# Kernel tuning notes

Measured on AMD Instinct MI355X. Metric: run time of the kernel, lower is better.

Reference implementation:

```python
import jax, jax.numpy as jnp
import numpy as np

N = 50000
E = 600000
IN_DIM = 256
H1, H2, H3 = 128, 64, 64
HEADS = 8


def _add_self_loops(edge_index, edge_weight=None):
    loop = jnp.arange(N, dtype=edge_index.dtype)
    src = jnp.concatenate([edge_index[0], loop])
    dst = jnp.concatenate([edge_index[1], loop])
    if edge_weight is None:
        return src, dst, None
    ew = jnp.concatenate([edge_weight, jnp.ones((N,), edge_weight.dtype)])
    return src, dst, ew


def gcn_conv(x, edge_index, edge_weight, W, b):
    # PyG GCNConv: add self-loops (weight 1), symmetric normalization, scatter-add.
    src, dst, ew = _add_self_loops(edge_index, edge_weight)
    deg = jax.ops.segment_sum(ew, dst, num_segments=N)          # [N]
    dinv = jnp.where(deg > 0, jax.lax.rsqrt(jnp.maximum(deg, 1e-12)), 0.0)
    coeff = dinv[src] * ew * dinv[dst]                          # [E+N]
    h = x @ W                                                    # [N, out]
    out = jax.ops.segment_sum(coeff[:, None] * h[src], dst, num_segments=N)
    return out + b


def gat_conv(x, edge_index, W, att_src, att_dst, b):
    # PyG GATConv, heads=HEADS, concat=False (mean over heads), leaky_relu slope 0.2.
    src, dst, _ = _add_self_loops(edge_index)
    C = W.shape[1] // HEADS
    h = (x @ W).reshape(N, HEADS, C)                             # [N,H,C]
    a_s = jnp.sum(h * att_src, axis=-1)                          # [N,H]
    a_d = jnp.sum(h * att_dst, axis=-1)                          # [N,H]
    e = jax.nn.leaky_relu(a_s[src] + a_d[dst], negative_slope=0.2)  # [E',H]
    # scatter-softmax over edges sharing a destination
    m = jax.ops.segment_max(e, dst, num_segments=N)              # [N,H]
    p = jnp.exp(e - m[dst])
    s = jax.ops.segment_sum(p, dst, num_segments=N)              # [N,H]
    alpha = p / (s[dst] + 1e-16)                                 # [E',H]
    out = jax.ops.segment_sum(alpha[:, :, None] * h[src], dst, num_segments=N)  # [N,H,C]
    return jnp.mean(out, axis=1) + b


def setup_inputs() -> dict:
    key = jax.random.key(0)
    ks = jax.random.split(key, 12)
    x = jax.random.normal(ks[0], (N, IN_DIM), dtype=jnp.float32)
    edge_index = jax.random.randint(ks[1], (2, E), 0, N, dtype=jnp.int32)
    edge_weight = jax.random.uniform(ks[2], (E,), dtype=jnp.float32)
    def glorot(k, shape):
        fan = shape[0] + shape[-1]
        return jax.random.normal(k, shape, dtype=jnp.float32) * np.sqrt(2.0 / fan)
    return {
        "x": x, "edge_index": edge_index, "edge_weight": edge_weight,
        "gc1_w": glorot(ks[3], (IN_DIM, H1)), "gc1_b": jnp.zeros((H1,), jnp.float32),
        "gat_w": glorot(ks[4], (H1, HEADS * H2)),
        "att_src": glorot(ks[5], (HEADS, H2)), "att_dst": glorot(ks[6], (HEADS, H2)),
        "gat_b": jnp.zeros((H2,), jnp.float32),
        "gc2_w": glorot(ks[7], (H2, H3)), "gc2_b": jnp.zeros((H3,), jnp.float32),
        "fc_w": glorot(ks[8], (H3, 1)), "fc_b": jnp.zeros((1,), jnp.float32),
    }


def reference(x, edge_index, edge_weight, gc1_w, gc1_b, gat_w, att_src, att_dst,
              gat_b, gc2_w, gc2_b, fc_w, fc_b):
    # dropout is inference no-op
    h = jax.nn.relu(gcn_conv(x, edge_index, edge_weight, gc1_w, gc1_b))
    h = jax.nn.relu(gat_conv(h, edge_index, gat_w, att_src, att_dst, gat_b))
    h = jax.nn.relu(gcn_conv(h, edge_index, edge_weight, gc2_w, gc2_b))
    return h @ fc_w + fc_b                                       # [N,1]
```

## Files before the change

kernel.cpp:

```cpp
#include <hip/hip_runtime.h>
#include <hip/hip_bf16.h>

#define GNN_N 50000
#define GNN_E 600000

typedef unsigned int uint;
typedef unsigned short ushort;
using short8 = __attribute__((ext_vector_type(8))) short;
using f32x4  = __attribute__((ext_vector_type(4))) float;

__device__ __forceinline__ float leaky02(float x) { return x > 0.f ? x : 0.2f * x; }
__device__ __forceinline__ ushort f2b(float f) {
    uint u = __float_as_uint(f);
    return (ushort)((u + 0x7fffu + ((u >> 16) & 1u)) >> 16);
}
__device__ __forceinline__ float b2f(ushort b) { return __uint_as_float(((uint)b) << 16); }

__global__ void gnn_hist(const int* __restrict__ dst, const float* __restrict__ ew,
                         int* __restrict__ cnt, float* __restrict__ deg, int e) {
    int i = blockIdx.x * blockDim.x + threadIdx.x;
    if (i >= e) return;
    int d = dst[i];
    atomicAdd(&cnt[d], 1);
    atomicAdd(&deg[d], ew[i]);
}
__global__ void gnn_deg_fin(float* deg, int n) {
    int i = blockIdx.x * blockDim.x + threadIdx.x;
    if (i < n) deg[i] = rsqrtf(1.0f + deg[i]);
}
__global__ void gnn_scan1(const int* __restrict__ cnt, int* __restrict__ row_ptr,
                          int* __restrict__ blksum, int n) {
    __shared__ int sh[256];
    int tid = threadIdx.x;
    int base = blockIdx.x * 1024 + tid * 4;
    int v0 = (base + 0 < n) ? cnt[base + 0] : 0;
    int v1 = (base + 1 < n) ? cnt[base + 1] : 0;
    int v2 = (base + 2 < n) ? cnt[base + 2] : 0;
    int v3 = (base + 3 < n) ? cnt[base + 3] : 0;
    int tsum = v0 + v1 + v2 + v3;
    sh[tid] = tsum;
    __syncthreads();
    for (int off = 1; off < 256; off <<= 1) {
        int t = (tid >= off) ? sh[tid - off] : 0;
        __syncthreads();
        sh[tid] += t;
        __syncthreads();
    }
    int excl = sh[tid] - tsum;
    if (base + 0 < n) row_ptr[base + 0] = excl; excl += v0;
    if (base + 1 < n) row_ptr[base + 1] = excl; excl += v1;
    if (base + 2 < n) row_ptr[base + 2] = excl; excl += v2;
    if (base + 3 < n) row_ptr[base + 3] = excl;
    if (tid == 255) blksum[blockIdx.x] = sh[255];
}
__global__ void gnn_scan2(int* blksum, int nblk, int* row_ptr_end, int total) {
    if (threadIdx.x == 0 && blockIdx.x == 0) {
        int run = 0;
        for (int b = 0; b < nblk; ++b) { int t = blksum[b]; blksum[b] = run; run += t; }
        *row_ptr_end = total;
    }
}
__global__ void gnn_scan3(int* row_ptr, const int* __restrict__ blksum, int n) {
    int i = blockIdx.x * blockDim.x + threadIdx.x;
    if (i < n) row_ptr[i] += blksum[i >> 10];
}
__global__ void gnn_scatter(const int* __restrict__ src, const int* __restrict__ dst,
                            const float* __restrict__ ew, const float* __restrict__ dinv,
                            const int* __restrict__ row_ptr, int* __restrict__ fill,
                            int* __restrict__ esrc, float* __restrict__ ecw, int e) {
    int i = blockIdx.x * blockDim.x + threadIdx.x;
    if (i >= e) return;
    int d = dst[i];
    int s = src[i];
    int pos = row_ptr[d] + atomicAdd(&fill[d], 1);
    esrc[pos] = s;
    ecw[pos] = dinv[s] * ew[i] * dinv[d];
}

__global__ void gnn_prep(const float* __restrict__ gc1_w, const float* __restrict__ gat_w,
                         const float* __restrict__ gc2_w, const float* __restrict__ att_src,
                         const float* __restrict__ att_dst, ushort* __restrict__ w1t,
                         ushort* __restrict__ w2t, ushort* __restrict__ w3t,
                         float* __restrict__ wa_t) {
    int t = blockIdx.x * 256 + threadIdx.x;
    if (t < 32768) {
        int k = t >> 7, n = t & 127;
        w1t[n * 256 + k] = f2b(gc1_w[t]);
        return;
    }
    t -= 32768;
    if (t < 65536) {
        int k = t >> 9, n = t & 511;
        w2t[n * 128 + k] = f2b(gat_w[t]);
        return;
    }
    t -= 65536;
    if (t < 4096) {
        int k = t >> 6, n = t & 63;
        w3t[n * 64 + k] = f2b(gc2_w[t]);
        return;
    }
    t -= 4096;
    if (t < 2048) {
        int j = t >> 7, k = t & 127;
        int h = j & 7;
        const float* av = (j < 8) ? att_src : att_dst;
        float s = 0.f;
        for (int c = 0; c < 64; ++c) s += gat_w[(size_t)k * 512 + h * 64 + c] * av[h * 64 + c];
        wa_t[j * 128 + k] = s;
    }
}

template <bool AF32>
__global__ __launch_bounds__(256) void gnn_mfma_gemm(const void* __restrict__ Av,
                                                     const ushort* __restrict__ Bt,
                                                     ushort* __restrict__ C,
                                                     int M, int N, int K) {
    __shared__ ushort As[64 * 40];
    __shared__ ushort Bs[64 * 40];
    const int tid = threadIdx.x;
    const int wv = tid >> 6, lane = tid & 63;
    const int g = lane >> 4, r = lane & 15;
    const int brow = blockIdx.y << 6, bcol = blockIdx.x << 6;

    const int srow = tid >> 2;
    const int skoff = (tid & 3) << 3;
    int arow = brow + srow;
    if (arow >= M) arow = M - 1;
    const ushort* A16 = (const ushort*)Av;
    const float*  A32 = (const float*)Av;
    const ushort* Ap16 = A16 + (size_t)arow * K + skoff;
    const float*  Ap32 = A32 + (size_t)arow * K + skoff;
    const ushort* Bp = Bt + (size_t)(bcol + srow) * K + skoff;
    ushort* AsW = &As[srow * 40 + skoff];
    ushort* BsW = &Bs[srow * 40 + skoff];

    f32x4 acc[4] = {};

    for (int k0 = 0; k0 < K; k0 += 32) {
        if constexpr (AF32) {
            float4 f0 = *(const float4*)(Ap32 + k0);
            float4 f1 = *(const float4*)(Ap32 + k0 + 4);
            short8 t;
            t[0] = (short)f2b(f0.x); t[1] = (short)f2b(f0.y);
            t[2] = (short)f2b(f0.z); t[3] = (short)f2b(f0.w);
            t[4] = (short)f2b(f1.x); t[5] = (short)f2b(f1.y);
            t[6] = (short)f2b(f1.z); t[7] = (short)f2b(f1.w);
            *(short8*)AsW = t;
        } else {
            *(short8*)AsW = *(const short8*)(Ap16 + k0);
        }
        *(short8*)BsW = *(const short8*)(Bp + k0);
        __syncthreads();
        short8 bfrag = *(const short8*)&Bs[(wv * 16 + r) * 40 + g * 8];
#pragma unroll
        for (int mb = 0; mb < 4; ++mb) {
            short8 afrag = *(const short8*)&As[(mb * 16 + r) * 40 + g * 8];
            acc[mb] = __builtin_amdgcn_mfma_f32_16x16x32_bf16(afrag, bfrag, acc[mb], 0, 0, 0);
        }
        __syncthreads();
    }

    const int col = bcol + wv * 16 + r;
#pragma unroll
    for (int mb = 0; mb < 4; ++mb) {
        int rowb = brow + mb * 16 + g * 4;
#pragma unroll
        for (int rr = 0; rr < 4; ++rr) {
            int row = rowb + rr;
            if (row < M) C[(size_t)row * N + col] = f2b(acc[mb][rr]);
        }
    }
}

__global__ __launch_bounds__(256) void gnn_gcn_node128_asd(const int* __restrict__ row_ptr,
                                                           const int* __restrict__ esrc,
                                                           const float* __restrict__ ecw,
                                                           const float* __restrict__ dinv,
                                                           const ushort* __restrict__ hb,
                                                           const float* __restrict__ b,
                                                           const float* __restrict__ wa,
                                                           ushort* __restrict__ out,
                                                           float* __restrict__ a_s,
                                                           float* __restrict__ a_d, int n) {
    __shared__ float swa[16 * 128];
    for (int i = threadIdx.x; i < 16 * 128; i += 256) swa[i] = wa[i];
    __syncthreads();
    int v = blockIdx.x * 4 + (threadIdx.x >> 6);
    int lane = threadIdx.x & 63;
    if (v >= n) return;
    float di = dinv[v];
    float sc = di * di;
    uint us = *(const uint*)(hb + (size_t)v * 128 + 2 * lane);
    float acc0 = sc * __uint_as_float(us << 16);
    float acc1 = sc * __uint_as_float(us & 0xffff0000u);
    int beg = row_ptr[v], end = row_ptr[v + 1];
    int p = beg;
    for (; p + 8 <= end; p += 8) {
        int s[8]; float c[8]; uint u[8];
#pragma unroll
        for (int t = 0; t < 8; ++t) s[t] = esrc[p + t];
#pragma unroll
        for (int t = 0; t < 8; ++t) c[t] = ecw[p + t];
#pragma unroll
        for (int t = 0; t < 8; ++t) u[t] = *(const uint*)(hb + (size_t)s[t] * 128 + 2 * lane);
#pragma unroll
        for (int t = 0; t < 8; ++t) {
            acc0 += c[t] * __uint_as_float(u[t] << 16);
            acc1 += c[t] * __uint_as_float(u[t] & 0xffff0000u);
        }
    }
    for (; p < end; ++p) {
        int s = esrc[p];
        float cw = ecw[p];
        uint u = *(const uint*)(hb + (size_t)s * 128 + 2 * lane);
        acc0 += cw * __uint_as_float(u << 16);
        acc1 += cw * __uint_as_float(u & 0xffff0000u);
    }
    float o0 = acc0 + b[2 * lane];
    float o1 = acc1 + b[2 * lane + 1];
    o0 = o0 > 0.f ? o0 : 0.f;
    o1 = o1 > 0.f ? o1 : 0.f;
    uint o = (uint)f2b(o0) | ((uint)f2b(o1) << 16);
    *(uint*)(out + (size_t)v * 128 + 2 * lane) = o;

    float part[16];
#pragma unroll
    for (int j = 0; j < 16; ++j)
        part[j] = o0 * swa[j * 128 + 2 * lane] + o1 * swa[j * 128 + 2 * lane + 1];
#pragma unroll
    for (int m = 1; m < 64; m <<= 1) {
#pragma unroll
        for (int j = 0; j < 16; ++j) part[j] += __shfl_xor(part[j], m);
    }
    if (lane == 0) {
#pragma unroll
        for (int j = 0; j < 8; ++j) {
            a_s[(size_t)v * 8 + j] = part[j];
            a_d[(size_t)v * 8 + j] = part[8 + j];
        }
    }
}

__global__ __launch_bounds__(256) void gnn_gat_node2(const int* __restrict__ row_ptr,
                                                     const int* __restrict__ esrc,
                                                     const float* __restrict__ a_s,
                                                     const float* __restrict__ a_d,
                                                     const ushort* __restrict__ h2,
                                                     const float* __restrict__ gat_b,
                                                     ushort* __restrict__ out, int n) {
    int v = blockIdx.x * 4 + (threadIdx.x >> 6);
    int lane = threadIdx.x & 63;
    if (v >= n) return;
    const int hd = lane >> 3;
    const float adh = a_d[(size_t)v * 8 + hd];

    float vh[8];
    float sl;
    {
        float ps = __expf(leaky02(a_s[(size_t)v * 8 + hd] + adh));
        short8 q = *(const short8*)(h2 + (size_t)v * 512 + lane * 8);
        sl = ps;
#pragma unroll
        for (int j = 0; j < 8; ++j) vh[j] = ps * b2f((ushort)q[j]);
    }
    int beg = row_ptr[v], end = row_ptr[v + 1];
    int p = beg;
    for (; p + 8 <= end; p += 8) {
        int s[8]; float e[8]; short8 q[8];
#pragma unroll
        for (int t = 0; t < 8; ++t) s[t] = esrc[p + t];
#pragma unroll
        for (int t = 0; t < 8; ++t) e[t] = a_s[(size_t)s[t] * 8 + hd];
#pragma unroll
        for (int t = 0; t < 8; ++t) q[t] = *(const short8*)(h2 + (size_t)s[t] * 512 + lane * 8);
#pragma unroll
        for (int t = 0; t < 8; ++t) {
            float pp = __expf(leaky02(e[t] + adh));
            sl += pp;
#pragma unroll
            for (int j = 0; j < 8; ++j) vh[j] += pp * b2f((ushort)q[t][j]);
        }
    }
    if (p + 4 <= end) {
        int s[4]; float e[4]; short8 q[4];
#pragma unroll
        for (int t = 0; t < 4; ++t) s[t] = esrc[p + t];
#pragma unroll
        for (int t = 0; t < 4; ++t) e[t] = a_s[(size_t)s[t] * 8 + hd];
#pragma unroll
        for (int t = 0; t < 4; ++t) q[t] = *(const short8*)(h2 + (size_t)s[t] * 512 + lane * 8);
#pragma unroll
        for (int t = 0; t < 4; ++t) {
            float pp = __expf(leaky02(e[t] + adh));
            sl += pp;
#pragma unroll
            for (int j = 0; j < 8; ++j) vh[j] += pp * b2f((ushort)q[t][j]);
        }
        p += 4;
    }
    for (; p < end; ++p) {
        int s = esrc[p];
        float pp = __expf(leaky02(a_s[(size_t)s * 8 + hd] + adh));
        short8 q = *(const short8*)(h2 + (size_t)s * 512 + lane * 8);
        sl += pp;
#pragma unroll
        for (int j = 0; j < 8; ++j) vh[j] += pp * b2f((ushort)q[j]);
    }
    float rs = 1.f / (sl + 1e-16f);
#pragma unroll
    for (int j = 0; j < 8; ++j) vh[j] *= rs;
#pragma unroll
    for (int m = 8; m < 64; m <<= 1) {
#pragma unroll
        for (int j = 0; j < 8; ++j) vh[j] += __shfl_xor(vh[j], m);
    }
    if (lane < 8) {
        short8 o;
#pragma unroll
        for (int j = 0; j < 8; ++j) {
            float t = 0.125f * vh[j] + gat_b[lane * 8 + j];
            t = t > 0.f ? t : 0.f;
            o[j] = (short)f2b(t);
        }
        *(short8*)(out + (size_t)v * 64 + lane * 8) = o;
    }
}

__global__ __launch_bounds__(256) void gnn_gcn_node64_fc(const int* __restrict__ row_ptr,
                                                         const int* __restrict__ esrc,
                                                         const float* __restrict__ ecw,
                                                         const float* __restrict__ dinv,
                                                         const ushort* __restrict__ hb,
                                                         const float* __restrict__ b,
                                                         const float* __restrict__ fc_w,
                                                         const float* __restrict__ fc_b,
                                                         float* __restrict__ out, int n) {
    int v = blockIdx.x * 4 + (threadIdx.x >> 6);
    int lane = threadIdx.x & 63;
    if (v >= n) return;
    float di = dinv[v];
    float acc = di * di * b2f(hb[(size_t)v * 64 + lane]);
    int beg = row_ptr[v], end = row_ptr[v + 1];
    int p = beg;
    for (; p + 8 <= end; p += 8) {
        int s[8]; float c[8]; ushort hv[8];
#pragma unroll
        for (int t = 0; t < 8; ++t) s[t] = esrc[p + t];
#pragma unroll
        for (int t = 0; t < 8; ++t) c[t] = ecw[p + t];
#pragma unroll
        for (int t = 0; t < 8; ++t) hv[t] = hb[(size_t)s[t] * 64 + lane];
#pragma unroll
        for (int t = 0; t < 8; ++t) acc += c[t] * b2f(hv[t]);
    }
    for (; p < end; ++p) {
        int s = esrc[p];
        acc += ecw[p] * b2f(hb[(size_t)s * 64 + lane]);
    }
    float o = acc + b[lane];
    o = o > 0.f ? o : 0.f;
    float val = o * fc_w[lane];
#pragma unroll
    for (int m = 32; m; m >>= 1) val += __shfl_xor(val, m);
    if (lane == 0) out[v] = val + fc_b[0];
}

extern "C" void kernel_launch(void* const* d_in, const int* in_sizes, int n_in,
                              void* d_out, int out_size, void* d_ws, size_t ws_size,
                              hipStream_t stream) {
    const float* x       = (const float*)d_in[0];
    const int*   ei      = (const int*)d_in[1];
    const float* ew      = (const float*)d_in[2];
    const float* gc1_w   = (const float*)d_in[3];
    const float* gc1_b   = (const float*)d_in[4];
    const float* gat_w   = (const float*)d_in[5];
    const float* att_src = (const float*)d_in[6];
    const float* att_dst = (const float*)d_in[7];
    const float* gat_b   = (const float*)d_in[8];
    const float* gc2_w   = (const float*)d_in[9];
    const float* gc2_b   = (const float*)d_in[10];
    const float* fc_w    = (const float*)d_in[11];
    const float* fc_b    = (const float*)d_in[12];
    float* out = (float*)d_out;

    const int N = GNN_N;
    const int E = in_sizes[2];
    const int* src = ei;
    const int* dst = ei + E;

    char* p = (char*)d_ws;
    ushort* h2b = (ushort*)p; p += (size_t)N * 512 * 2;
    ushort* h1b = (ushort*)p; p += (size_t)N * 128 * 2;
    ushort* g1b = (ushort*)p; p += (size_t)N * 128 * 2;
    ushort* g2b = (ushort*)p; p += (size_t)N * 64 * 2;
    ushort* h3b = (ushort*)p; p += (size_t)N * 64 * 2;
    ushort* w1t = (ushort*)p; p += (size_t)128 * 256 * 2;
    ushort* w2t = (ushort*)p; p += (size_t)512 * 128 * 2;
    ushort* w3t = (ushort*)p; p += (size_t)64 * 64 * 2;
    float*  wa_t = (float*)p; p += 16 * 128 * 4;
    float*  a_s = (float*)p;  p += (size_t)N * 8 * 4;
    float*  a_d = (float*)p;  p += (size_t)N * 8 * 4;
    int* row_ptr = (int*)p;   p += (size_t)(N + 64) * 4;
    int* esrc = (int*)p;      p += (size_t)E * 4;
    float* ecw = (float*)p;   p += (size_t)E * 4;
    int* cnt = (int*)p;       p += (size_t)N * 4;
    int* fill = (int*)p;      p += (size_t)N * 4;
    float* dinv = (float*)p;  p += (size_t)N * 4;
    int* blksum = (int*)p;    p += 4096;

    auto cdiv = [](long a, long b) { return (int)((a + b - 1) / b); };

    hipMemsetAsync(cnt, 0, (size_t)N * 12, stream);
    gnn_hist<<<cdiv(E, 256), 256, 0, stream>>>(dst, ew, cnt, dinv, E);
    gnn_deg_fin<<<cdiv(N, 256), 256, 0, stream>>>(dinv, N);
    const int nblk = cdiv(N, 1024);
    gnn_scan1<<<nblk, 256, 0, stream>>>(cnt, row_ptr, blksum, N);
    gnn_scan2<<<1, 64, 0, stream>>>(blksum, nblk, row_ptr + N, E);
    gnn_scan3<<<cdiv(N, 256), 256, 0, stream>>>(row_ptr, blksum, N);
    gnn_scatter<<<cdiv(E, 256), 256, 0, stream>>>(src, dst, ew, dinv, row_ptr, fill, esrc, ecw, E);

    gnn_prep<<<408, 256, 0, stream>>>(gc1_w, gat_w, gc2_w, att_src, att_dst, w1t, w2t, w3t, wa_t);

    {
        dim3 grid(128 / 64, cdiv(N, 64));
        gnn_mfma_gemm<true><<<grid, 256, 0, stream>>>(x, w1t, h1b, N, 128, 256);
    }
    gnn_gcn_node128_asd<<<cdiv(N, 4), 256, 0, stream>>>(row_ptr, esrc, ecw, dinv, h1b, gc1_b,
                                                        wa_t, g1b, a_s, a_d, N);

    {
        dim3 grid(512 / 64, cdiv(N, 64));
        gnn_mfma_gemm<false><<<grid, 256, 0, stream>>>(g1b, w2t, h2b, N, 512, 128);
    }
    gnn_gat_node2<<<cdiv(N, 4), 256, 0, stream>>>(row_ptr, esrc, a_s, a_d, h2b, gat_b, g2b, N);

    {
        dim3 grid(1, cdiv(N, 64));
        gnn_mfma_gemm<false><<<grid, 256, 0, stream>>>(g2b, w3t, h3b, N, 64, 64);
    }
    gnn_gcn_node64_fc<<<cdiv(N, 4), 256, 0, stream>>>(row_ptr, esrc, ecw, dinv, h3b, gc2_b,
                                                      fc_w, fc_b, out, N);
}
```

Measured before the change: 374.9 us.

## Aggregate GAT over 128-dim inputs before projection, then fused GEMM with head-mean

Reorders the GAT layer so attention-weighted aggregation runs on the 128-wide g1 features per head, producing an 8x128 per-node tensor z. A single GEMM with K=1024 then applies the per-head weights, pre-scaled by 1/8 for the head mean, and fuses bias and ReLU into its epilogue. This drops the 512-wide h2 GEMM and its per-edge gathers of 1 KB rows in exchange for 256-byte gathers, at the cost of writing and reading a 2 KB-per-node z buffer and a larger-K GEMM.

Result: faster. 348.1 us (-7.2%).

```diff
diff --git a/kernel.cpp b/kernel.cpp
--- a/kernel.cpp
+++ b/kernel.cpp
@@ -80,7 +80,7 @@
 __global__ void gnn_prep(const float* __restrict__ gc1_w, const float* __restrict__ gat_w,
                          const float* __restrict__ gc2_w, const float* __restrict__ att_src,
                          const float* __restrict__ att_dst, ushort* __restrict__ w1t,
-                         ushort* __restrict__ w2t, ushort* __restrict__ w3t,
+                         ushort* __restrict__ w2s_t, ushort* __restrict__ w3t,
                          float* __restrict__ wa_t) {
     int t = blockIdx.x * 256 + threadIdx.x;
     if (t < 32768) {
@@ -90,8 +90,9 @@
     }
     t -= 32768;
     if (t < 65536) {
-        int k = t >> 9, n = t & 511;
-        w2t[n * 128 + k] = f2b(gat_w[t]);
+        int c = t >> 10, r = t & 1023;
+        int h = r >> 7, k = r & 127;
+        w2s_t[t] = f2b(0.125f * gat_w[(size_t)k * 512 + h * 64 + c]);
         return;
     }
     t -= 65536;
@@ -111,10 +112,11 @@
     }
 }
 
-template <bool AF32>
+template <bool AF32, bool BIAS>
 __global__ __launch_bounds__(256) void gnn_mfma_gemm(const void* __restrict__ Av,
                                                      const ushort* __restrict__ Bt,
                                                      ushort* __restrict__ C,
+                                                     const float* __restrict__ bias,
                                                      int M, int N, int K) {
     __shared__ ushort As[64 * 40];
     __shared__ ushort Bs[64 * 40];
@@ -162,13 +164,22 @@
     }
 
     const int col = bcol + wv * 16 + r;
+    float bv = 0.f;
+    if constexpr (BIAS) bv = bias[col];
 #pragma unroll
     for (int mb = 0; mb < 4; ++mb) {
         int rowb = brow + mb * 16 + g * 4;
 #pragma unroll
         for (int rr = 0; rr < 4; ++rr) {
             int row = rowb + rr;
-            if (row < M) C[(size_t)row * N + col] = f2b(acc[mb][rr]);
+            if (row < M) {
+                float val = acc[mb][rr];
+                if constexpr (BIAS) {
+                    val += bv;
+                    val = val > 0.f ? val : 0.f;
+                }
+                C[(size_t)row * N + col] = f2b(val);
+            }
         }
     }
 }
@@ -242,88 +253,74 @@
     }
 }
 
-__global__ __launch_bounds__(256) void gnn_gat_node2(const int* __restrict__ row_ptr,
-                                                     const int* __restrict__ esrc,
-                                                     const float* __restrict__ a_s,
-                                                     const float* __restrict__ a_d,
-                                                     const ushort* __restrict__ h2,
-                                                     const float* __restrict__ gat_b,
-                                                     ushort* __restrict__ out, int n) {
+__global__ __launch_bounds__(256) void gnn_gat_z(const int* __restrict__ row_ptr,
+                                                 const int* __restrict__ esrc,
+                                                 const float* __restrict__ a_s,
+                                                 const float* __restrict__ a_d,
+                                                 const ushort* __restrict__ g1b,
+                                                 ushort* __restrict__ zb, int n) {
     int v = blockIdx.x * 4 + (threadIdx.x >> 6);
     int lane = threadIdx.x & 63;
     if (v >= n) return;
-    const int hd = lane >> 3;
-    const float adh = a_d[(size_t)v * 8 + hd];
-
-    float vh[8];
+    const int hh = lane & 7;
+    const float adh = a_d[(size_t)v * 8 + hh];
+
+    float z0[8] = {}, z1[8] = {};
     float sl;
     {
-        float ps = __expf(leaky02(a_s[(size_t)v * 8 + hd] + adh));
-        short8 q = *(const short8*)(h2 + (size_t)v * 512 + lane * 8);
-        sl = ps;
-#pragma unroll
-        for (int j = 0; j < 8; ++j) vh[j] = ps * b2f((ushort)q[j]);
+        float pv = __expf(leaky02(a_s[(size_t)v * 8 + hh] + adh));
+        uint u = *(const uint*)(g1b + (size_t)v * 128 + 2 * lane);
+        float g0 = __uint_as_float(u << 16);
+        float g1v = __uint_as_float(u & 0xffff0000u);
+        sl = pv;
+        float ph[8];
+#pragma unroll
+        for (int h = 0; h < 8; ++h) ph[h] = __shfl(pv, h);
+#pragma unroll
+        for (int h = 0; h < 8; ++h) { z0[h] += ph[h] * g0; z1[h] += ph[h] * g1v; }
     }
     int beg = row_ptr[v], end = row_ptr[v + 1];
     int p = beg;
-    for (; p + 8 <= end; p += 8) {
-        int s[8]; float e[8]; short8 q[8];
-#pragma unroll
-        for (int t = 0; t < 8; ++t) s[t] = esrc[p + t];
-#pragma unroll
-        for (int t = 0; t < 8; ++t) e[t] = a_s[(size_t)s[t] * 8 + hd];
-#pragma unroll
-        for (int t = 0; t < 8; ++t) q[t] = *(const short8*)(h2 + (size_t)s[t] * 512 + lane * 8);
-#pragma unroll
-        for (int t = 0; t < 8; ++t) {
-            float pp = __expf(leaky02(e[t] + adh));
-            sl += pp;
-#pragma unroll
-            for (int j = 0; j < 8; ++j) vh[j] += pp * b2f((ushort)q[t][j]);
-        }
-    }
-    if (p + 4 <= end) {
-        int s[4]; float e[4]; short8 q[4];
+    for (; p + 4 <= end; p += 4) {
+        int s[4]; float e[4]; uint u[4];
 #pragma unroll
         for (int t = 0; t < 4; ++t) s[t] = esrc[p + t];
 #pragma unroll
-        for (int t = 0; t < 4; ++t) e[t] = a_s[(size_t)s[t] * 8 + hd];
-#pragma unroll
-        for (int t = 0; t < 4; ++t) q[t] = *(const short8*)(h2 + (size_t)s[t] * 512 + lane * 8);
+        for (int t = 0; t < 4; ++t) e[t] = a_s[(size_t)s[t] * 8 + hh];
+#pragma unroll
+        for (int t = 0; t < 4; ++t) u[t] = *(const uint*)(g1b + (size_t)s[t] * 128 + 2 * lane);
 #pragma unroll
         for (int t = 0; t < 4; ++t) {
-            float pp = __expf(leaky02(e[t] + adh));
-            sl += pp;
-#pragma unroll
-            for (int j = 0; j < 8; ++j) vh[j] += pp * b2f((ushort)q[t][j]);
-        }
-        p += 4;
+            float pv = __expf(leaky02(e[t] + adh));
+            sl += pv;
+            float g0 = __uint_as_float(u[t] << 16);
+            float g1v = __uint_as_float(u[t] & 0xffff0000u);
+            float ph[8];
+#pragma unroll
+            for (int h = 0; h < 8; ++h) ph[h] = __shfl(pv, h);
+#pragma unroll
+            for (int h = 0; h < 8; ++h) { z0[h] += ph[h] * g0; z1[h] += ph[h] * g1v; }
+        }
     }
     for (; p < end; ++p) {
         int s = esrc[p];
-        float pp = __expf(leaky02(a_s[(size_t)s * 8 + hd] + adh));
-        short8 q = *(const short8*)(h2 + (size_t)s * 512 + lane * 8);
-        sl += pp;
-#pragma unroll
-        for (int j = 0; j < 8; ++j) vh[j] += pp * b2f((ushort)q[j]);
-    }
-    float rs = 1.f / (sl + 1e-16f);
-#pragma unroll
-    for (int j = 0; j < 8; ++j) vh[j] *= rs;
-#pragma unroll
-    for (int m = 8; m < 64; m <<= 1) {
-#pragma unroll
-        for (int j = 0; j < 8; ++j) vh[j] += __shfl_xor(vh[j], m);
-    }
-    if (lane < 8) {
-        short8 o;
-#pragma unroll
-        for (int j = 0; j < 8; ++j) {
-            float t = 0.125f * vh[j] + gat_b[lane * 8 + j];
-            t = t > 0.f ? t : 0.f;
-            o[j] = (short)f2b(t);
-        }
-        *(short8*)(out + (size_t)v * 64 + lane * 8) = o;
+        float pv = __expf(leaky02(a_s[(size_t)s * 8 + hh] + adh));
+        uint u = *(const uint*)(g1b + (size_t)s * 128 + 2 * lane);
+        sl += pv;
+        float g0 = __uint_as_float(u << 16);
+        float g1v = __uint_as_float(u & 0xffff0000u);
+        float ph[8];
+#pragma unroll
+        for (int h = 0; h < 8; ++h) ph[h] = __shfl(pv, h);
+#pragma unroll
+        for (int h = 0; h < 8; ++h) { z0[h] += ph[h] * g0; z1[h] += ph[h] * g1v; }
+    }
+    float slx = sl + 1e-16f;
+#pragma unroll
+    for (int h = 0; h < 8; ++h) {
+        float rs = 1.f / __shfl(slx, h);
+        uint o = (uint)f2b(z0[h] * rs) | ((uint)f2b(z1[h] * rs) << 16);
+        *(uint*)(zb + (size_t)v * 1024 + h * 128 + 2 * lane) = o;
     }
 }
 
@@ -390,13 +387,13 @@
     const int* dst = ei + E;
 
     char* p = (char*)d_ws;
-    ushort* h2b = (ushort*)p; p += (size_t)N * 512 * 2;
+    ushort* zb  = (ushort*)p; p += (size_t)N * 1024 * 2;
     ushort* h1b = (ushort*)p; p += (size_t)N * 128 * 2;
     ushort* g1b = (ushort*)p; p += (size_t)N * 128 * 2;
     ushort* g2b = (ushort*)p; p += (size_t)N * 64 * 2;
     ushort* h3b = (ushort*)p; p += (size_t)N * 64 * 2;
     ushort* w1t = (ushort*)p; p += (size_t)128 * 256 * 2;
-    ushort* w2t = (ushort*)p; p += (size_t)512 * 128 * 2;
+    ushort* w2s_t = (ushort*)p; p += (size_t)64 * 1024 * 2;
     ushort* w3t = (ushort*)p; p += (size_t)64 * 64 * 2;
     float*  wa_t = (float*)p; p += 16 * 128 * 4;
     float*  a_s = (float*)p;  p += (size_t)N * 8 * 4;
@@ -420,24 +417,24 @@
     gnn_scan3<<<cdiv(N, 256), 256, 0, stream>>>(row_ptr, blksum, N);
     gnn_scatter<<<cdiv(E, 256), 256, 0, stream>>>(src, dst, ew, dinv, row_ptr, fill, esrc, ecw, E);
 
-    gnn_prep<<<408, 256, 0, stream>>>(gc1_w, gat_w, gc2_w, att_src, att_dst, w1t, w2t, w3t, wa_t);
+    gnn_prep<<<408, 256, 0, stream>>>(gc1_w, gat_w, gc2_w, att_src, att_dst, w1t, w2s_t, w3t, wa_t);
 
     {
         dim3 grid(128 / 64, cdiv(N, 64));
-        gnn_mfma_gemm<true><<<grid, 256, 0, stream>>>(x, w1t, h1b, N, 128, 256);
+        gnn_mfma_gemm<true, false><<<grid, 256, 0, stream>>>(x, w1t, h1b, nullptr, N, 128, 256);
     }
     gnn_gcn_node128_asd<<<cdiv(N, 4), 256, 0, stream>>>(row_ptr, esrc, ecw, dinv, h1b, gc1_b,
                                                         wa_t, g1b, a_s, a_d, N);
 
-    {
-        dim3 grid(512 / 64, cdiv(N, 64));
-        gnn_mfma_gemm<false><<<grid, 256, 0, stream>>>(g1b, w2t, h2b, N, 512, 128);
-    }
-    gnn_gat_node2<<<cdiv(N, 4), 256, 0, stream>>>(row_ptr, esrc, a_s, a_d, h2b, gat_b, g2b, N);
-
+    gnn_gat_z<<<cdiv(N, 4), 256, 0, stream>>>(row_ptr, esrc, a_s, a_d, g1b, zb, N);
     {
         dim3 grid(1, cdiv(N, 64));
-        gnn_mfma_gemm<false><<<grid, 256, 0, stream>>>(g2b, w3t, h3b, N, 64, 64);
+        gnn_mfma_gemm<false, true><<<grid, 256, 0, stream>>>(zb, w2s_t, g2b, gat_b, N, 64, 1024);
+    }
+
+    {
+        dim3 grid(1, cdiv(N, 64));
+        gnn_mfma_gemm<false, false><<<grid, 256, 0, stream>>>(g2b, w3t, h3b, nullptr, N, 64, 64);
     }
     gnn_gcn_node64_fc<<<cdiv(N, 4), 256, 0, stream>>>(row_ptr, esrc, ecw, dinv, h3b, gc2_b,
                                                       fc_w, fc_b, out, N);
```
